# Performance work log

Hardware: AMD Instinct MI355X
Metric: run time of the kernel (lower is better)

The kernel has to match this reference:

```python
import jax, jax.numpy as jnp
import numpy as np

B, L = 64, 16384
INTERP_FACTOR = 0.25
WINDOW, STEP = 256, 64
ALPHA, BETA, TEMP = 0.12, 0.9, 1.0
A = -0.75  # PyTorch grid_sample bicubic coefficient


def _cubic_w(t):
    # cubic convolution kernel (Keys, a=-0.75), matches torch bicubic
    at = jnp.abs(t)
    w_near = ((A + 2.0) * at - (A + 3.0)) * at * at + 1.0          # |t| <= 1
    w_far = ((A * at - 5.0 * A) * at + 8.0 * A) * at - 4.0 * A      # 1 < |t| < 2
    return jnp.where(at <= 1.0, w_near, jnp.where(at < 2.0, w_far, 0.0))


def cubic_interpolate_1d(signal, interp_factor):
    # equivalent to the grid_sample(mode='bicubic', padding='border',
    # align_corners=True) hack on a (B,1,1,n) image: y-direction is identity.
    b, n = signal.shape
    num_points = int((n - 1) / interp_factor) + 1
    x = jnp.linspace(0.0, 1.0, num_points) * (n - 1)                 # sample coords
    i0 = jnp.floor(x).astype(jnp.int32)
    frac = x - i0.astype(x.dtype)
    offs = jnp.arange(-1, 3)                                         # 4 taps
    idx = jnp.clip(i0[:, None] + offs[None, :], 0, n - 1)            # (P,4) border pad
    w = _cubic_w(frac[:, None] - offs[None, :].astype(x.dtype))      # (P,4)
    taps = signal[:, idx]                                            # (B,P,4)
    return jnp.einsum('bpk,pk->bp', taps, w)


def _apply_kernels(x):
    # gamma-normalized mix: 0.5*polynomial(deg=2,off=1.3) + 0.5*gaussian(c=0.7,s=1.0)
    poly = (x + 1.3) ** 2
    gauss = jnp.exp(-0.5 * ((x - 0.7) / 1.0) ** 2)
    return 0.5 * poly + 0.5 * gauss


def soft_minimum(a, b, temperature):
    b = jnp.broadcast_to(b, a.shape)
    stacked = jnp.stack([-a * temperature, -b * temperature], axis=0)
    return -jax.nn.logsumexp(stacked, axis=0) / temperature


def _forward(signal):
    interp = cubic_interpolate_1d(signal, INTERP_FACTOR)             # (B, n)
    n = interp.shape[1]
    n_windows = (n - WINDOW) // STEP + 1
    starts = jnp.arange(n_windows) * STEP
    idx = starts[:, None] + jnp.arange(WINDOW)[None, :]              # (nw, W)
    windows = interp[:, idx]                                         # (B, nw, W)
    kw = _apply_kernels(windows)                                     # per-window kernel eval
    M = jnp.abs(jnp.fft.fft(kw, axis=-1))                            # magnitude spectrum
    Mmax = jnp.max(M, axis=-1, keepdims=True)
    thr = ALPHA * Mmax                                               # local threshold
    mask = jax.nn.sigmoid((M - thr) * TEMP)                          # soft threshold
    Mt = M * mask
    return soft_minimum(Mt, BETA * Mmax, TEMP)                       # smart min (B, nw, W)


def setup_inputs() -> dict:
    key = jax.random.key(0)
    return {"signal": jax.random.normal(key, (B, L), dtype=jnp.float32)}


def reference(signal):
    return _forward(signal)
```

## Files before the change

kernel.cpp:

```cpp
#include <hip/hip_runtime.h>
#include <math.h>

#define LSIG 16384
#define NWIN 1020
#define WTILE 32
#define MTILES 32
#define STRIP 576
#define RBSTRIDE 260
#define RBOFF (STRIP * 8)
#define PMAXOFF (RBOFF + 16 * RBSTRIDE * 4)
#define LDSBYTES (PMAXOFF + 32 * 4 * 4)

typedef __attribute__((ext_vector_type(8))) short short8;
typedef __attribute__((ext_vector_type(4))) float f32x4;
typedef __attribute__((ext_vector_type(4))) unsigned short us4;

__device__ __forceinline__ unsigned short f2b(float f) {
    union { float f; unsigned int u; } x; x.f = f;
    unsigned int r = x.u + 0x7fffu + ((x.u >> 16) & 1u);
    return (unsigned short)(r >> 16);
}

__device__ __forceinline__ float kwf(float x) {
    float p = x + 1.3f;
    float d = x - 0.7f;
    return fmaf(0.5f * p, p, 0.5f * __expf(-0.5f * d * d));
}

__device__ __forceinline__ float smin_fast(float Mv, float thr, float bb) {
    float t = __expf(thr - Mv);
    float Mt = Mv * __builtin_amdgcn_rcpf(1.0f + t);
    return fminf(Mt, bb);
}

__global__ void build_dft(unsigned short* __restrict__ Bf) {
    const int t = blockIdx.x;
    const int c = threadIdx.x;
    const int bin = ((c >> 6) << 5) + (((c >> 5) & 1) << 4) + (c & 15);
    const int kind = (c >> 4) & 1;
    float v;
    if (c == 16) {
        v = (t & 1) ? -1.0f : 1.0f;
    } else {
        const int prod = (bin * t) & 255;
        const float a = (float)prod * 0.024543692606170f;
        v = (kind == 0) ? __cosf(a) : -__sinf(a);
    }
    Bf[(((t >> 3) * 256) + c) * 8 + (t & 7)] = f2b(v);
}

__global__ __launch_bounds__(256, 8) void ntfa_gemm(const float* __restrict__ sig,
                                                    const unsigned short* __restrict__ Bf,
                                                    float* __restrict__ out) {
    __shared__ __align__(16) char lds[LDSBYTES];
    float* rb = (float*)(lds + RBOFF);
    float* pmax_s = (float*)(lds + PMAXOFF);

    const int tid = threadIdx.x;
    const int lane = tid & 63;
    const int wid = tid >> 6;
    const int wn0 = wid * 64;
    const int lm = lane & 15;
    const int lg = lane >> 4;
    const bool spec = (wid == 0) && (lm == 0);

    const int mtile = blockIdx.x;
    const int b = blockIdx.y;
    const int S0q = mtile * 512;
    const float* srow = sig + (size_t)b * LSIG;

#pragma unroll
    for (int k = 0; k < 3; ++k) {
        int q = tid + k * 256;
        if (q < STRIP) {
            int gq = S0q + q;
            float o0 = 0.f, o1 = 0.f, o2 = 0.f, o3 = 0.f;
            if (gq <= 16383) {
                float ta = srow[gq - 1 < 0 ? 0 : gq - 1];
                float tb = srow[gq];
                float tc = srow[gq + 1 > 16383 ? 16383 : gq + 1];
                float td = srow[gq + 2 > 16383 ? 16383 : gq + 2];
                float x0 = tb;
                float x1 = fmaf(ta, -0.10546875f, fmaf(tb, 0.87890625f,
                            fmaf(tc, 0.26171875f, td * -0.03515625f)));
                float x2 = fmaf(ta, -0.09375f, fmaf(tb, 0.59375f,
                            fmaf(tc, 0.59375f, td * -0.09375f)));
                float x3 = fmaf(ta, -0.03515625f, fmaf(tb, 0.26171875f,
                            fmaf(tc, 0.87890625f, td * -0.10546875f)));
                o0 = kwf(x0); o1 = kwf(x1); o2 = kwf(x2); o3 = kwf(x3);
                if (gq == 16383) { o1 = 0.f; o2 = 0.f; o3 = 0.f; }
            }
            us4 pk; pk.x = f2b(o0); pk.y = f2b(o1); pk.z = f2b(o2); pk.w = f2b(o3);
            int la = q * 8;
            la ^= ((la >> 7) & 7) << 4;
            *(us4*)(lds + la) = pk;
        }
    }
    __syncthreads();

    f32x4 acc[2][4] = {};
#pragma unroll
    for (int ks = 0; ks < 8; ++ks) {
        short8 afr[2];
#pragma unroll
        for (int mt = 0; mt < 2; ++mt) {
            int sb = ((mt * 16 + lm) * 64 + ks * 32 + lg * 8) * 2;
            sb ^= ((sb >> 7) & 7) << 4;
            afr[mt] = *(const short8*)(lds + sb);
        }
#pragma unroll
        for (int np = 0; np < 2; ++np) {
            short8 bp0 = *(const short8*)(Bf + ((ks * 4 + lg) * 256 + wn0 + (2 * np) * 16 + lm) * 8);
            short8 bp1 = *(const short8*)(Bf + ((ks * 4 + lg) * 256 + wn0 + (2 * np + 1) * 16 + lm) * 8);
            acc[0][2 * np]     = __builtin_amdgcn_mfma_f32_16x16x32_bf16(afr[0], bp0, acc[0][2 * np], 0, 0, 0);
            acc[0][2 * np + 1] = __builtin_amdgcn_mfma_f32_16x16x32_bf16(afr[0], bp1, acc[0][2 * np + 1], 0, 0, 0);
            acc[1][2 * np]     = __builtin_amdgcn_mfma_f32_16x16x32_bf16(afr[1], bp0, acc[1][2 * np], 0, 0, 0);
            acc[1][2 * np + 1] = __builtin_amdgcn_mfma_f32_16x16x32_bf16(afr[1], bp1, acc[1][2 * np + 1], 0, 0, 0);
        }
    }

    float M[2][2][4], M128[2][4], pm[2][4];
#pragma unroll
    for (int mt = 0; mt < 2; ++mt) {
#pragma unroll
        for (int k = 0; k < 2; ++k)
#pragma unroll
            for (int r = 0; r < 4; ++r) {
                float re = acc[mt][2 * k][r];
                float im = acc[mt][2 * k + 1][r];
                if (k == 0 && spec) {
                    M[mt][0][r] = fabsf(re);
                    M128[mt][r] = fabsf(im);
                } else {
                    M[mt][k][r] = __builtin_amdgcn_sqrtf(fmaf(re, re, im * im));
                }
            }
#pragma unroll
        for (int r = 0; r < 4; ++r) {
            float p = fmaxf(M[mt][0][r], M[mt][1][r]);
            if (spec) p = fmaxf(p, M128[mt][r]);
            pm[mt][r] = p;
        }
    }
#pragma unroll
    for (int msk = 1; msk < 16; msk <<= 1)
#pragma unroll
        for (int mt = 0; mt < 2; ++mt)
#pragma unroll
            for (int r = 0; r < 4; ++r)
                pm[mt][r] = fmaxf(pm[mt][r], __shfl_xor(pm[mt][r], msk));

    if (lm == 0) {
#pragma unroll
        for (int mt = 0; mt < 2; ++mt)
#pragma unroll
            for (int r = 0; r < 4; ++r)
                pmax_s[(mt * 16 + lg * 4 + r) * 4 + wid] = pm[mt][r];
    }
    __syncthreads();

    const int w0 = mtile * WTILE;
#pragma unroll
    for (int mt = 0; mt < 2; ++mt) {
#pragma unroll
        for (int r = 0; r < 4; ++r) {
            const int win16 = lg * 4 + r;
            const float* pp = pmax_s + (mt * 16 + win16) * 4;
            const float Mx = fmaxf(fmaxf(pp[0], pp[1]), fmaxf(pp[2], pp[3]));
            const float thr = 0.12f * Mx;
            const float bb = 0.9f * Mx;
            float* row = rb + win16 * RBSTRIDE;
#pragma unroll
            for (int k = 0; k < 2; ++k) {
                const int bin = wid * 32 + k * 16 + lm;
                const float outv = smin_fast(M[mt][k][r], thr, bb);
                row[bin] = outv;
                row[256 - bin] = outv;
                if (k == 0 && spec)
                    row[128] = smin_fast(M128[mt][r], thr, bb);
            }
        }
        __syncthreads();
        {
            const int r16 = lane >> 4;
            const int f4c = lane & 15;
            const int win16s = wid * 4 + r16;
            const int gw = w0 + mt * 16 + win16s;
            if (gw < NWIN) {
                const float* rrow = rb + win16s * RBSTRIDE;
                float* orow = out + (((size_t)(b * NWIN + gw)) << 8);
#pragma unroll
                for (int it = 0; it < 4; ++it) {
                    const int c4 = f4c + it * 16;
                    f32x4 v = *(const f32x4*)(rrow + c4 * 4);
                    __builtin_nontemporal_store(v, (f32x4*)(orow + c4 * 4));
                }
            }
        }
        __syncthreads();
    }
}

extern "C" void kernel_launch(void* const* d_in, const int* in_sizes, int n_in,
                              void* d_out, int out_size, void* d_ws, size_t ws_size,
                              hipStream_t stream) {
    const float* sig = (const float*)d_in[0];
    float* out = (float*)d_out;
    unsigned short* Bf = (unsigned short*)d_ws;

    hipLaunchKernelGGL(build_dft, dim3(256), dim3(256), 0, stream, Bf);
    hipLaunchKernelGGL(ntfa_gemm, dim3(MTILES, 64), dim3(256), 0, stream, sig, Bf, out);
}
```

Baseline: 30.22 us.

## Process each M-subtile's GEMM and epilogue sequentially to cut accumulator registers

The two 16-row M subtiles are now handled one after another: each runs its MFMA loop, then its magnitude, max-reduction, soft-min and store epilogue, before the next one starts. This halves the live accumulator and magnitude registers, shrinks the per-window max buffer in LDS, and drops the trailing barrier. It is meant to ease register pressure and let the second subtile's GEMM overlap with the first subtile's stores. The cost is that the DFT B fragments are fetched from global memory twice instead of once.

```diff
diff --git a/kernel.cpp b/kernel.cpp
--- a/kernel.cpp
+++ b/kernel.cpp
@@ -9,7 +9,7 @@
 #define RBSTRIDE 260
 #define RBOFF (STRIP * 8)
 #define PMAXOFF (RBOFF + 16 * RBSTRIDE * 4)
-#define LDSBYTES (PMAXOFF + 32 * 4 * 4)
+#define LDSBYTES (PMAXOFF + 16 * 4 * 4)
 
 typedef __attribute__((ext_vector_type(8))) short short8;
 typedef __attribute__((ext_vector_type(4))) float f32x4;
@@ -98,74 +98,62 @@
     }
     __syncthreads();
 
-    f32x4 acc[2][4] = {};
-#pragma unroll
-    for (int ks = 0; ks < 8; ++ks) {
-        short8 afr[2];
-#pragma unroll
-        for (int mt = 0; mt < 2; ++mt) {
+    const int w0 = mtile * WTILE;
+
+#pragma unroll
+    for (int mt = 0; mt < 2; ++mt) {
+        f32x4 acc[4] = {};
+#pragma unroll
+        for (int ks = 0; ks < 8; ++ks) {
             int sb = ((mt * 16 + lm) * 64 + ks * 32 + lg * 8) * 2;
             sb ^= ((sb >> 7) & 7) << 4;
-            afr[mt] = *(const short8*)(lds + sb);
-        }
-#pragma unroll
-        for (int np = 0; np < 2; ++np) {
-            short8 bp0 = *(const short8*)(Bf + ((ks * 4 + lg) * 256 + wn0 + (2 * np) * 16 + lm) * 8);
-            short8 bp1 = *(const short8*)(Bf + ((ks * 4 + lg) * 256 + wn0 + (2 * np + 1) * 16 + lm) * 8);
-            acc[0][2 * np]     = __builtin_amdgcn_mfma_f32_16x16x32_bf16(afr[0], bp0, acc[0][2 * np], 0, 0, 0);
-            acc[0][2 * np + 1] = __builtin_amdgcn_mfma_f32_16x16x32_bf16(afr[0], bp1, acc[0][2 * np + 1], 0, 0, 0);
-            acc[1][2 * np]     = __builtin_amdgcn_mfma_f32_16x16x32_bf16(afr[1], bp0, acc[1][2 * np], 0, 0, 0);
-            acc[1][2 * np + 1] = __builtin_amdgcn_mfma_f32_16x16x32_bf16(afr[1], bp1, acc[1][2 * np + 1], 0, 0, 0);
-        }
-    }
-
-    float M[2][2][4], M128[2][4], pm[2][4];
-#pragma unroll
-    for (int mt = 0; mt < 2; ++mt) {
+            const short8 afr = *(const short8*)(lds + sb);
+#pragma unroll
+            for (int np = 0; np < 2; ++np) {
+                short8 bp0 = *(const short8*)(Bf + ((ks * 4 + lg) * 256 + wn0 + (2 * np) * 16 + lm) * 8);
+                short8 bp1 = *(const short8*)(Bf + ((ks * 4 + lg) * 256 + wn0 + (2 * np + 1) * 16 + lm) * 8);
+                acc[2 * np]     = __builtin_amdgcn_mfma_f32_16x16x32_bf16(afr, bp0, acc[2 * np], 0, 0, 0);
+                acc[2 * np + 1] = __builtin_amdgcn_mfma_f32_16x16x32_bf16(afr, bp1, acc[2 * np + 1], 0, 0, 0);
+            }
+        }
+
+        float M[2][4], M128v[4], pm[4];
 #pragma unroll
         for (int k = 0; k < 2; ++k)
 #pragma unroll
             for (int r = 0; r < 4; ++r) {
-                float re = acc[mt][2 * k][r];
-                float im = acc[mt][2 * k + 1][r];
+                float re = acc[2 * k][r];
+                float im = acc[2 * k + 1][r];
                 if (k == 0 && spec) {
-                    M[mt][0][r] = fabsf(re);
-                    M128[mt][r] = fabsf(im);
+                    M[0][r] = fabsf(re);
+                    M128v[r] = fabsf(im);
                 } else {
-                    M[mt][k][r] = __builtin_amdgcn_sqrtf(fmaf(re, re, im * im));
+                    M[k][r] = __builtin_amdgcn_sqrtf(fmaf(re, re, im * im));
                 }
             }
 #pragma unroll
         for (int r = 0; r < 4; ++r) {
-            float p = fmaxf(M[mt][0][r], M[mt][1][r]);
-            if (spec) p = fmaxf(p, M128[mt][r]);
-            pm[mt][r] = p;
-        }
-    }
-#pragma unroll
-    for (int msk = 1; msk < 16; msk <<= 1)
-#pragma unroll
-        for (int mt = 0; mt < 2; ++mt)
+            float p = fmaxf(M[0][r], M[1][r]);
+            if (spec) p = fmaxf(p, M128v[r]);
+            pm[r] = p;
+        }
+#pragma unroll
+        for (int msk = 1; msk < 16; msk <<= 1)
 #pragma unroll
             for (int r = 0; r < 4; ++r)
-                pm[mt][r] = fmaxf(pm[mt][r], __shfl_xor(pm[mt][r], msk));
-
-    if (lm == 0) {
-#pragma unroll
-        for (int mt = 0; mt < 2; ++mt)
+                pm[r] = fmaxf(pm[r], __shfl_xor(pm[r], msk));
+
+        if (lm == 0) {
 #pragma unroll
             for (int r = 0; r < 4; ++r)
-                pmax_s[(mt * 16 + lg * 4 + r) * 4 + wid] = pm[mt][r];
-    }
-    __syncthreads();
-
-    const int w0 = mtile * WTILE;
-#pragma unroll
-    for (int mt = 0; mt < 2; ++mt) {
+                pmax_s[(lg * 4 + r) * 4 + wid] = pm[r];
+        }
+        __syncthreads();
+
 #pragma unroll
         for (int r = 0; r < 4; ++r) {
             const int win16 = lg * 4 + r;
-            const float* pp = pmax_s + (mt * 16 + win16) * 4;
+            const float* pp = pmax_s + win16 * 4;
             const float Mx = fmaxf(fmaxf(pp[0], pp[1]), fmaxf(pp[2], pp[3]));
             const float thr = 0.12f * Mx;
             const float bb = 0.9f * Mx;
@@ -173,11 +161,11 @@
 #pragma unroll
             for (int k = 0; k < 2; ++k) {
                 const int bin = wid * 32 + k * 16 + lm;
-                const float outv = smin_fast(M[mt][k][r], thr, bb);
+                const float outv = smin_fast(M[k][r], thr, bb);
                 row[bin] = outv;
                 row[256 - bin] = outv;
                 if (k == 0 && spec)
-                    row[128] = smin_fast(M128[mt][r], thr, bb);
+                    row[128] = smin_fast(M128v[r], thr, bb);
             }
         }
         __syncthreads();
@@ -197,7 +185,6 @@
                 }
             }
         }
-        __syncthreads();
     }
 }
 
```

New measurement: 36.36 us. 1.2x slower.
